# Performance work log

Hardware: AMD Instinct MI355X
Metric: run time of the kernel (lower is better)

## Reference

```python
import jax, jax.numpy as jnp
import numpy as np


def setup_inputs() -> dict:
    key = jax.random.key(0)
    k1, k2 = jax.random.split(key)
    B, N, M = 8, 8192, 8192
    pred = jax.random.normal(k1, (B, N, 3), dtype=jnp.float32)
    gt = jax.random.normal(k2, (B, M, 3), dtype=jnp.float32)
    return {"pred": pred, "gt": gt}


def _chamfer(pred, gt):
    # pred: [B,N,3], gt: [B,M,3]
    # squared pairwise distances: ||p||^2 + ||q||^2 - 2 p.q  -> [B,N,M]
    p_sq = jnp.sum(pred * pred, axis=-1)           # [B,N]
    q_sq = jnp.sum(gt * gt, axis=-1)               # [B,M]
    cross = jnp.einsum('bnd,bmd->bnm', pred, gt)   # [B,N,M]
    dist = p_sq[:, :, None] + q_sq[:, None, :] - 2.0 * cross
    dist = jnp.maximum(dist, 0.0)  # numerical floor, distances are non-negative
    # kaolin chamfer_distance: mean over points of nearest-neighbor sq-dist, both sides
    p2q = jnp.mean(jnp.min(dist, axis=2), axis=1)  # [B]
    q2p = jnp.mean(jnp.min(dist, axis=1), axis=1)  # [B]
    chamfer = p2q + q2p                            # [B] (w1 = w2 = 1)
    return jnp.mean(chamfer)                       # scalar, torch.mean over batch


def reference(pred, gt):
    return _chamfer(pred, gt)
```

## Files before the change

kernel.cpp:

```cpp
#include <hip/hip_runtime.h>


typedef short bf16x8 __attribute__((ext_vector_type(8)));
typedef float f32x16 __attribute__((ext_vector_type(16)));

#define B_SZ   8
#define NPTS   8192
#define TOTAL  (B_SZ * NPTS)
#define BLOCK  256
#define SLICE  1024
#define SPLITS (NPTS / SLICE)
#define TILES  (SLICE / 32)
#define RED_GRID 128

__device__ __forceinline__ unsigned short bf16rn(float f, float* rem) {
    unsigned u = __float_as_uint(f);
    unsigned h = (u + 0x8000u) & 0xFFFF0000u;
    *rem = f - __uint_as_float(h);
    return (unsigned short)(h >> 16);
}

__global__ __launch_bounds__(BLOCK) void chamfer_prep_mfma(
    const float* __restrict__ gt, const float* __restrict__ pred,
    uint4* __restrict__ TgA, uint4* __restrict__ TgB, float* __restrict__ Wg,
    uint4* __restrict__ TpA, uint4* __restrict__ TpB, float* __restrict__ Wp)
{
    int i = blockIdx.x * BLOCK + threadIdx.x;
    const float* src = blockIdx.y ? pred : gt;
    uint4* TA = blockIdx.y ? TpA : TgA;
    uint4* TB = blockIdx.y ? TpB : TgB;
    float* W  = blockIdx.y ? Wp  : Wg;

    float x = src[3 * (size_t)i + 0];
    float y = src[3 * (size_t)i + 1];
    float z = src[3 * (size_t)i + 2];
    float w = fmaf(x, x, fmaf(y, y, z * z));
    W[i] = w;

    float ux = -2.f * x, uy = -2.f * y, uz = -2.f * z;
    float rx, ry, rz, dx, dy, dz, rw1, rw2, rw3;
    unsigned short uhx = bf16rn(ux, &rx), uhy = bf16rn(uy, &ry), uhz = bf16rn(uz, &rz);
    unsigned short ulx = bf16rn(rx, &dx), uly = bf16rn(ry, &dy), ulz = bf16rn(rz, &dz);
    unsigned short wh = bf16rn(w, &rw1), wm = bf16rn(rw1, &rw2), wl = bf16rn(rw2, &rw3);
    union { unsigned short s[16]; uint4 v[2]; } A;
    A.s[0] = uhx; A.s[1] = uhy; A.s[2]  = uhz;
    A.s[3] = uhx; A.s[4] = uhy; A.s[5]  = uhz;
    A.s[6] = ulx; A.s[7] = uly; A.s[8]  = ulz;
    A.s[9] = ulx; A.s[10] = uly; A.s[11] = ulz;
    A.s[12] = wh; A.s[13] = wm; A.s[14] = wl; A.s[15] = 0;
    TA[2 * (size_t)i]     = A.v[0];
    TA[2 * (size_t)i + 1] = A.v[1];

    float sx, sy, sz, ex, ey, ez;
    unsigned short qhx = bf16rn(x, &sx), qhy = bf16rn(y, &sy), qhz = bf16rn(z, &sz);
    unsigned short qlx = bf16rn(sx, &ex), qly = bf16rn(sy, &ey), qlz = bf16rn(sz, &ez);
    union { unsigned short s[16]; uint4 v[2]; } Bb;
    Bb.s[0] = qhx; Bb.s[1] = qhy; Bb.s[2]  = qhz;
    Bb.s[3] = qlx; Bb.s[4] = qly; Bb.s[5]  = qlz;
    Bb.s[6] = qhx; Bb.s[7] = qhy; Bb.s[8]  = qhz;
    Bb.s[9] = qlx; Bb.s[10] = qly; Bb.s[11] = qlz;
    Bb.s[12] = 0x3F80; Bb.s[13] = 0x3F80; Bb.s[14] = 0x3F80; Bb.s[15] = 0;
    TB[2 * (size_t)i]     = Bb.v[0];
    TB[2 * (size_t)i + 1] = Bb.v[1];
}

__global__ __launch_bounds__(BLOCK, 3) void chamfer_nn_mfma(
    const uint4* __restrict__ TgA, const uint4* __restrict__ TpB,
    const float* __restrict__ Wp, unsigned* __restrict__ minP,
    const uint4* __restrict__ TpA, const uint4* __restrict__ TgB,
    const float* __restrict__ Wg, unsigned* __restrict__ minG)
{
    __shared__ uint4 tileU[SLICE * 2];
    char* tileC = (char*)tileU;

    const int qb  = blockIdx.x;
    const int b   = blockIdx.y;
    const int dir = blockIdx.z >> 3;
    const int s   = blockIdx.z & 7;
    const int t    = threadIdx.x;
    const int lane = t & 63, wid = t >> 6;
    const int col  = lane & 31, hi = lane >> 5;

    const uint4* TA      = dir ? TpA : TgA;
    const uint4* TB      = dir ? TgB : TpB;
    const float* WQ      = dir ? Wg  : Wp;
    unsigned*    minbuf  = dir ? minG : minP;

    const uint4* srcA = TA + ((size_t)b * NPTS + (size_t)s * SLICE) * 2;
    for (int it = 0; it < (SLICE * 2) / BLOCK; ++it) {
        int g = t + it * BLOCK;
        uint4 v = srcA[g];
        int tl = g >> 1, gh = g & 1;
        int off = (tl * 32 + gh * 16) ^ (((tl >> 2) & 7) << 4);
        *(uint4*)(tileC + off) = v;
    }

    const int qblk = qb * 256 + wid * 64;
    const char* TBc = (const char*)(TB + ((size_t)b * NPTS + qblk) * 2);
    bf16x8 bq0 = *(const bf16x8*)(TBc + (size_t)col * 32 + hi * 16);
    bf16x8 bq1 = *(const bf16x8*)(TBc + (size_t)(col + 32) * 32 + hi * 16);

    f32x16 zacc;
#pragma unroll
    for (int j = 0; j < 16; ++j) zacc[j] = 0.f;

    float m0 = 3.0e38f, m1 = 3.0e38f;
    __syncthreads();

    const int hi16 = hi * 16;
#pragma unroll 2
    for (int tt = 0; tt < TILES; ++tt) {
        int trow = tt * 32 + col;
        int off = (trow * 32 + hi16) ^ (((trow >> 2) & 7) << 4);
        bf16x8 a = *(const bf16x8*)(tileC + off);
        f32x16 d0 = __builtin_amdgcn_mfma_f32_32x32x16_bf16(a, bq0, zacc, 0, 0, 0);
        f32x16 d1 = __builtin_amdgcn_mfma_f32_32x32x16_bf16(a, bq1, zacc, 0, 0, 0);
        float u0 = fminf(fminf(fminf(d0[0], d0[1]), fminf(d0[2], d0[3])),
                         fminf(fminf(d0[4], d0[5]), fminf(d0[6], d0[7])));
        float v0 = fminf(fminf(fminf(d0[8], d0[9]), fminf(d0[10], d0[11])),
                         fminf(fminf(d0[12], d0[13]), fminf(d0[14], d0[15])));
        m0 = fminf(m0, fminf(u0, v0));
        float u1 = fminf(fminf(fminf(d1[0], d1[1]), fminf(d1[2], d1[3])),
                         fminf(fminf(d1[4], d1[5]), fminf(d1[6], d1[7])));
        float v1 = fminf(fminf(fminf(d1[8], d1[9]), fminf(d1[10], d1[11])),
                         fminf(fminf(d1[12], d1[13]), fminf(d1[14], d1[15])));
        m1 = fminf(m1, fminf(u1, v1));
    }

    m0 = fminf(m0, __shfl_xor(m0, 32));
    m1 = fminf(m1, __shfl_xor(m1, 32));
    if (lane < 32) {
        int q0 = b * NPTS + qblk + lane;
        float d0f = fmaxf(m0 + WQ[q0], 0.f);
        atomicMin(&minbuf[q0], __float_as_uint(d0f));
        int q1 = q0 + 32;
        float d1f = fmaxf(m1 + WQ[q1], 0.f);
        atomicMin(&minbuf[q1], __float_as_uint(d1f));
    }
}

__global__ __launch_bounds__(BLOCK) void chamfer_reduce_mfma(
    const float* __restrict__ a, int na,
    const float* __restrict__ b, int nb,
    float* __restrict__ out, float sa, float sb)
{
    __shared__ float part[BLOCK / 64];
    float s = 0.f;
    int tid = blockIdx.x * BLOCK + threadIdx.x;
    int stride = gridDim.x * BLOCK;
    const float4* a4 = (const float4*)a;
    for (int i = tid; i < na / 4; i += stride) {
        float4 v = a4[i];
        s += (v.x + v.y + v.z + v.w) * sa;
    }
    const float4* b4 = (const float4*)b;
    for (int i = tid; i < nb / 4; i += stride) {
        float4 v = b4[i];
        s += (v.x + v.y + v.z + v.w) * sb;
    }
    for (int o = 32; o > 0; o >>= 1) s += __shfl_down(s, o, 64);
    int w = threadIdx.x >> 6;
    if ((threadIdx.x & 63) == 0) part[w] = s;
    __syncthreads();
    if (threadIdx.x == 0) {
        float tot = 0.f;
#pragma unroll
        for (int i = 0; i < BLOCK / 64; ++i) tot += part[i];
        atomicAdd(out, tot);
    }
}

extern "C" void kernel_launch(void* const* d_in, const int* in_sizes, int n_in,
                              void* d_out, int out_size, void* d_ws, size_t ws_size,
                              hipStream_t stream) {
    const float* pred = (const float*)d_in[0];
    const float* gt   = (const float*)d_in[1];
    float* out = (float*)d_out;

    char* ws = (char*)d_ws;
    uint4* TgA = (uint4*)(ws);
    uint4* TpA = (uint4*)(ws + (size_t)TOTAL * 32);
    uint4* TgB = (uint4*)(ws + (size_t)TOTAL * 64);
    uint4* TpB = (uint4*)(ws + (size_t)TOTAL * 96);
    float* Wg  = (float*)(ws + (size_t)TOTAL * 128);
    float* Wp  = (float*)(ws + (size_t)TOTAL * 128 + (size_t)TOTAL * 4);
    unsigned* minP = (unsigned*)(ws + (size_t)TOTAL * 128 + (size_t)TOTAL * 8);
    unsigned* minG = (unsigned*)(ws + (size_t)TOTAL * 128 + (size_t)TOTAL * 12);

    hipMemsetAsync(minP, 0x7f, (size_t)TOTAL * 8, stream);
    hipMemsetAsync(out, 0, sizeof(float), stream);

    chamfer_prep_mfma<<<dim3(TOTAL / BLOCK, 2), BLOCK, 0, stream>>>(
        gt, pred, TgA, TgB, Wg, TpA, TpB, Wp);

    chamfer_nn_mfma<<<dim3(NPTS / 256, B_SZ, 2 * SPLITS), BLOCK, 0, stream>>>(
        TgA, TpB, Wp, minP, TpA, TgB, Wg, minG);

    chamfer_reduce_mfma<<<RED_GRID, BLOCK, 0, stream>>>(
        (const float*)minP, TOTAL, (const float*)minG, TOTAL, out,
        1.0f / (float)TOTAL, 1.0f / (float)TOTAL);
}
```

Measured before the change: 117.1 us.

## Fuse NN search and reduction by looping all reference slices per block

Each block now walks all reference slices itself, staging one 1024-point tile into LDS per pass, rather than being split across 8 slice-blocks that combine results through atomicMin. This removes the min buffers, their memset, the atomicMin traffic and the separate reduction kernel, since each block reduces its final minima and atomically adds into the output. It also simplifies LDS address computation and the min-reduction tree. The trade-off is a grid cut to 512 blocks with serialized load/sync phases and no overlap between tile loads and MFMA work, plus lower occupancy (launch bound 2).

Result: faster. 99.64 us (-14.9%).

```diff
diff --git a/kernel.cpp b/kernel.cpp
--- a/kernel.cpp
+++ b/kernel.cpp
@@ -8,10 +8,10 @@
 #define NPTS   8192
 #define TOTAL  (B_SZ * NPTS)
 #define BLOCK  256
+#define QB     256
 #define SLICE  1024
-#define SPLITS (NPTS / SLICE)
+#define NSTAGE (NPTS / SLICE)
 #define TILES  (SLICE / 32)
-#define RED_GRID 128
 
 __device__ __forceinline__ unsigned short bf16rn(float f, float* rem) {
     unsigned u = __float_as_uint(f);
@@ -64,38 +64,37 @@
     TB[2 * (size_t)i + 1] = Bb.v[1];
 }
 
-__global__ __launch_bounds__(BLOCK, 3) void chamfer_nn_mfma(
+__device__ __forceinline__ float minred(f32x16 d, float m) {
+    float r0 = fminf(fminf(d[0], d[1]), d[2]);
+    float r1 = fminf(fminf(d[3], d[4]), d[5]);
+    float r2 = fminf(fminf(d[6], d[7]), d[8]);
+    float r3 = fminf(fminf(d[9], d[10]), d[11]);
+    float r4 = fminf(fminf(d[12], d[13]), d[14]);
+    float s0 = fminf(fminf(r0, r1), r2);
+    float s1 = fminf(fminf(r3, r4), d[15]);
+    return fminf(fminf(m, s0), s1);
+}
+
+__global__ __launch_bounds__(BLOCK, 2) void chamfer_nn_fused(
     const uint4* __restrict__ TgA, const uint4* __restrict__ TpB,
-    const float* __restrict__ Wp, unsigned* __restrict__ minP,
+    const float* __restrict__ Wp,
     const uint4* __restrict__ TpA, const uint4* __restrict__ TgB,
-    const float* __restrict__ Wg, unsigned* __restrict__ minG)
+    const float* __restrict__ Wg,
+    float* __restrict__ out)
 {
     __shared__ uint4 tileU[SLICE * 2];
+    __shared__ float psum[4];
     char* tileC = (char*)tileU;
 
-    const int qb  = blockIdx.x;
-    const int b   = blockIdx.y;
-    const int dir = blockIdx.z >> 3;
-    const int s   = blockIdx.z & 7;
-    const int t    = threadIdx.x;
-    const int lane = t & 63, wid = t >> 6;
-    const int col  = lane & 31, hi = lane >> 5;
+    const int qb = blockIdx.x, b = blockIdx.y, dir = blockIdx.z;
+    const int t = threadIdx.x, lane = t & 63, wid = t >> 6;
+    const int col = lane & 31, hi = lane >> 5;
 
-    const uint4* TA      = dir ? TpA : TgA;
-    const uint4* TB      = dir ? TgB : TpB;
-    const float* WQ      = dir ? Wg  : Wp;
-    unsigned*    minbuf  = dir ? minG : minP;
+    const uint4* TA = dir ? TpA : TgA;
+    const uint4* TB = dir ? TgB : TpB;
+    const float* WQ = dir ? Wg  : Wp;
 
-    const uint4* srcA = TA + ((size_t)b * NPTS + (size_t)s * SLICE) * 2;
-    for (int it = 0; it < (SLICE * 2) / BLOCK; ++it) {
-        int g = t + it * BLOCK;
-        uint4 v = srcA[g];
-        int tl = g >> 1, gh = g & 1;
-        int off = (tl * 32 + gh * 16) ^ (((tl >> 2) & 7) << 4);
-        *(uint4*)(tileC + off) = v;
-    }
-
-    const int qblk = qb * 256 + wid * 64;
+    const int qblk = qb * QB + wid * 64;
     const char* TBc = (const char*)(TB + ((size_t)b * NPTS + qblk) * 2);
     bf16x8 bq0 = *(const bf16x8*)(TBc + (size_t)col * 32 + hi * 16);
     bf16x8 bq1 = *(const bf16x8*)(TBc + (size_t)(col + 32) * 32 + hi * 16);
@@ -103,70 +102,44 @@
     f32x16 zacc;
 #pragma unroll
     for (int j = 0; j < 16; ++j) zacc[j] = 0.f;
+    float m0 = 3.0e38f, m1 = 3.0e38f;
+    const int abase = (col * 32 + hi * 16) ^ (((col >> 2) & 7) << 4);
 
-    float m0 = 3.0e38f, m1 = 3.0e38f;
-    __syncthreads();
+    for (int st = 0; st < NSTAGE; ++st) {
+        const uint4* srcA = TA + ((size_t)b * NPTS + (size_t)st * SLICE) * 2;
+#pragma unroll
+        for (int it = 0; it < (SLICE * 2) / BLOCK; ++it) {
+            int g = t + it * BLOCK;
+            uint4 v = srcA[g];
+            int tl = g >> 1, gh = g & 1;
+            int off = (tl * 32 + gh * 16) ^ (((tl >> 2) & 7) << 4);
+            *(uint4*)(tileC + off) = v;
+        }
+        __syncthreads();
 
-    const int hi16 = hi * 16;
 #pragma unroll 2
-    for (int tt = 0; tt < TILES; ++tt) {
-        int trow = tt * 32 + col;
-        int off = (trow * 32 + hi16) ^ (((trow >> 2) & 7) << 4);
-        bf16x8 a = *(const bf16x8*)(tileC + off);
-        f32x16 d0 = __builtin_amdgcn_mfma_f32_32x32x16_bf16(a, bq0, zacc, 0, 0, 0);
-        f32x16 d1 = __builtin_amdgcn_mfma_f32_32x32x16_bf16(a, bq1, zacc, 0, 0, 0);
-        float u0 = fminf(fminf(fminf(d0[0], d0[1]), fminf(d0[2], d0[3])),
-                         fminf(fminf(d0[4], d0[5]), fminf(d0[6], d0[7])));
-        float v0 = fminf(fminf(fminf(d0[8], d0[9]), fminf(d0[10], d0[11])),
-                         fminf(fminf(d0[12], d0[13]), fminf(d0[14], d0[15])));
-        m0 = fminf(m0, fminf(u0, v0));
-        float u1 = fminf(fminf(fminf(d1[0], d1[1]), fminf(d1[2], d1[3])),
-                         fminf(fminf(d1[4], d1[5]), fminf(d1[6], d1[7])));
-        float v1 = fminf(fminf(fminf(d1[8], d1[9]), fminf(d1[10], d1[11])),
-                         fminf(fminf(d1[12], d1[13]), fminf(d1[14], d1[15])));
-        m1 = fminf(m1, fminf(u1, v1));
+        for (int tt = 0; tt < TILES; ++tt) {
+            bf16x8 a = *(const bf16x8*)(tileC + abase + tt * 1024);
+            f32x16 d0 = __builtin_amdgcn_mfma_f32_32x32x16_bf16(a, bq0, zacc, 0, 0, 0);
+            m0 = minred(d0, m0);
+            f32x16 d1 = __builtin_amdgcn_mfma_f32_32x32x16_bf16(a, bq1, zacc, 0, 0, 0);
+            m1 = minred(d1, m1);
+        }
+        __syncthreads();
     }
 
     m0 = fminf(m0, __shfl_xor(m0, 32));
     m1 = fminf(m1, __shfl_xor(m1, 32));
-    if (lane < 32) {
-        int q0 = b * NPTS + qblk + lane;
-        float d0f = fmaxf(m0 + WQ[q0], 0.f);
-        atomicMin(&minbuf[q0], __float_as_uint(d0f));
-        int q1 = q0 + 32;
-        float d1f = fmaxf(m1 + WQ[q1], 0.f);
-        atomicMin(&minbuf[q1], __float_as_uint(d1f));
-    }
-}
-
-__global__ __launch_bounds__(BLOCK) void chamfer_reduce_mfma(
-    const float* __restrict__ a, int na,
-    const float* __restrict__ b, int nb,
-    float* __restrict__ out, float sa, float sb)
-{
-    __shared__ float part[BLOCK / 64];
-    float s = 0.f;
-    int tid = blockIdx.x * BLOCK + threadIdx.x;
-    int stride = gridDim.x * BLOCK;
-    const float4* a4 = (const float4*)a;
-    for (int i = tid; i < na / 4; i += stride) {
-        float4 v = a4[i];
-        s += (v.x + v.y + v.z + v.w) * sa;
-    }
-    const float4* b4 = (const float4*)b;
-    for (int i = tid; i < nb / 4; i += stride) {
-        float4 v = b4[i];
-        s += (v.x + v.y + v.z + v.w) * sb;
-    }
-    for (int o = 32; o > 0; o >>= 1) s += __shfl_down(s, o, 64);
-    int w = threadIdx.x >> 6;
-    if ((threadIdx.x & 63) == 0) part[w] = s;
+    float wq = WQ[(size_t)b * NPTS + qb * QB + t];
+    float d = fmaxf((lane < 32 ? m0 : m1) + wq, 0.0f);
+    float s = d;
+#pragma unroll
+    for (int o = 1; o < 64; o <<= 1) s += __shfl_xor(s, o);
+    if (lane == 0) psum[wid] = s;
     __syncthreads();
-    if (threadIdx.x == 0) {
-        float tot = 0.f;
-#pragma unroll
-        for (int i = 0; i < BLOCK / 64; ++i) tot += part[i];
-        atomicAdd(out, tot);
+    if (t == 0) {
+        float tot = (psum[0] + psum[1]) + (psum[2] + psum[3]);
+        atomicAdd(out, tot * (1.0f / (float)TOTAL));
     }
 }
 
@@ -184,19 +157,12 @@
     uint4* TpB = (uint4*)(ws + (size_t)TOTAL * 96);
     float* Wg  = (float*)(ws + (size_t)TOTAL * 128);
     float* Wp  = (float*)(ws + (size_t)TOTAL * 128 + (size_t)TOTAL * 4);
-    unsigned* minP = (unsigned*)(ws + (size_t)TOTAL * 128 + (size_t)TOTAL * 8);
-    unsigned* minG = (unsigned*)(ws + (size_t)TOTAL * 128 + (size_t)TOTAL * 12);
 
-    hipMemsetAsync(minP, 0x7f, (size_t)TOTAL * 8, stream);
     hipMemsetAsync(out, 0, sizeof(float), stream);
 
     chamfer_prep_mfma<<<dim3(TOTAL / BLOCK, 2), BLOCK, 0, stream>>>(
         gt, pred, TgA, TgB, Wg, TpA, TpB, Wp);
 
-    chamfer_nn_mfma<<<dim3(NPTS / 256, B_SZ, 2 * SPLITS), BLOCK, 0, stream>>>(
-        TgA, TpB, Wp, minP, TpA, TgB, Wg, minG);
-
-    chamfer_reduce_mfma<<<RED_GRID, BLOCK, 0, stream>>>(
-        (const float*)minP, TOTAL, (const float*)minG, TOTAL, out,
-        1.0f / (float)TOTAL, 1.0f / (float)TOTAL);
+    chamfer_nn_fused<<<dim3(NPTS / QB, B_SZ, 2), BLOCK, 0, stream>>>(
+        TgA, TpB, Wp, TpA, TgB, Wg, out);
 }
```
